# Kernel tuning notes

Hardware: AMD Instinct MI355X
Metric: run time of the kernel (lower is better)

Reference implementation:

```python
import jax, jax.numpy as jnp
import numpy as np

MARGIN = 0.3
N, D = 8192, 128
NUM_CLASSES = 512


def setup_inputs() -> dict:
    key = jax.random.key(0)
    k1, k2 = jax.random.split(key)
    embeddings = jax.random.normal(k1, (N, D), dtype=jnp.float32)
    targets = jax.random.randint(k2, (N,), 0, NUM_CLASSES, dtype=jnp.int64)
    return {"embeddings": embeddings, "targets": targets}


def reference(embeddings, targets):
    x = embeddings.astype(jnp.float32)
    # pairwise squared-euclidean: ||xi||^2 + ||xj||^2 - 2 xi.xj, clamped then sqrt
    sq = jnp.sum(x * x, axis=1)  # [N]
    dist = sq[:, None] + sq[None, :] - 2.0 * (x @ x.T)
    dist = jnp.sqrt(jnp.clip(dist, 1e-12, None))  # [N, N]

    is_pos = targets[:, None] == targets[None, :]  # includes diagonal, as in torch code

    # batch-hard mining: per-row hardest positive (max) and hardest negative (min)
    dist_ap = jnp.max(jnp.where(is_pos, dist, -jnp.inf), axis=1)
    dist_an = jnp.min(jnp.where(is_pos, jnp.inf, dist), axis=1)

    # MarginRankingLoss(margin)(dist_an, dist_ap, y=1) = mean(relu(margin - (dist_an - dist_ap)))
    loss = jnp.mean(jax.nn.relu(dist_ap - dist_an + MARGIN))
    return loss
```

## Files before the change

### kernel.cpp

```cpp
#include <hip/hip_runtime.h>
#include <hip/hip_bf16.h>

#define N_ROWS 8192
#define DIM 128
#define MARGIN_F 0.3f

typedef __attribute__((ext_vector_type(8))) short short8;
typedef __attribute__((ext_vector_type(4))) float f32x4;
typedef __attribute__((ext_vector_type(4))) int int4v;

typedef const void __attribute__((address_space(1)))* gas1_t;
typedef void __attribute__((address_space(3)))* las3_t;

__device__ __forceinline__ void load_lds16(const void* g, void* l) {
  __builtin_amdgcn_global_load_lds((gas1_t)g, (las3_t)l, 16, 0, 0);
}

__global__ __launch_bounds__(256) void prep_kernel(
    const float* __restrict__ x, const int* __restrict__ tgt,
    unsigned short* __restrict__ xb, float2* __restrict__ meta,
    int* __restrict__ apb, int* __restrict__ anb) {
  const int w = threadIdx.x >> 6, l = threadIdx.x & 63;
  const int row = blockIdx.x * 4 + w;
  const float2* xp = reinterpret_cast<const float2*>(x + (size_t)row * DIM);
  float2 v = xp[l];
  __hip_bfloat16 b0 = __float2bfloat16(v.x);
  __hip_bfloat16 b1 = __float2bfloat16(v.y);
  ushort2 st;
  st.x = *reinterpret_cast<unsigned short*>(&b0);
  st.y = *reinterpret_cast<unsigned short*>(&b1);
  reinterpret_cast<ushort2*>(xb)[(size_t)row * 64 + l] = st;
  float s = v.x * v.x + v.y * v.y;
  #pragma unroll
  for (int off = 32; off >= 1; off >>= 1) s += __shfl_xor(s, off);
  if (l == 0) {
    float2 m;
    m.x = s;
    m.y = __int_as_float(tgt[row]);
    meta[row] = m;
    apb[row] = 0x00000000;
    anb[row] = 0x7f800000;
  }
}

__global__ __launch_bounds__(256, 4) void gram_mine_kernel(
    const unsigned short* __restrict__ xb, const float2* __restrict__ meta,
    int* __restrict__ apb, int* __restrict__ anb) {
  __shared__ unsigned short Bs[2][64 * 128];

  const int t = threadIdx.x;
  const int w = t >> 6, l = t & 63;
  const int l15 = l & 15, l4 = l >> 4;
  const int rb = blockIdx.x * 128 + w * 32;
  const int chunkbase = blockIdx.y * 512;

  short8 a[2][4];
  #pragma unroll
  for (int rf = 0; rf < 2; ++rf) {
    const short8* p = reinterpret_cast<const short8*>(xb + (size_t)(rb + rf * 16 + l15) * DIM);
    #pragma unroll
    for (int kk = 0; kk < 4; ++kk) a[rf][kk] = p[kk * 4 + l4];
  }
  int t_r[8];
  #pragma unroll
  for (int rf = 0; rf < 2; ++rf)
    #pragma unroll
    for (int rg = 0; rg < 4; ++rg)
      t_r[rf * 4 + rg] = __float_as_int(meta[rb + rf * 16 + l4 * 4 + rg].y);

  float ap2[8], an2[8];
  #pragma unroll
  for (int i = 0; i < 8; ++i) { ap2[i] = -__builtin_inff(); an2[i] = __builtin_inff(); }

  auto stage = [&](int buf, int ct) {
    const int colbase = chunkbase + ct * 64;
    #pragma unroll
    for (int r = 0; r < 4; ++r) {
      int c = r * 256 + t;
      int col_local = c >> 4;
      int off = ((c & 15) * 16) ^ ((col_local & 7) << 4);
      const char* src = reinterpret_cast<const char*>(xb) +
                        (size_t)(colbase + col_local) * 256 + off;
      load_lds16(src, (char*)(&Bs[buf][0]) + c * 16);
    }
  };

  stage(0, 0);
  int cur = 0;
  for (int ct = 0; ct < 8; ++ct) {
    __syncthreads();
    if (ct < 7) stage(cur ^ 1, ct + 1);

    const int colbase = chunkbase + ct * 64;
    float sqc[4]; int tc[4];
    #pragma unroll
    for (int cf = 0; cf < 4; ++cf) {
      float2 m = meta[colbase + cf * 16 + l15];
      sqc[cf] = m.x; tc[cf] = __float_as_int(m.y);
    }

    f32x4 acc[2][4];
    #pragma unroll
    for (int rf = 0; rf < 2; ++rf)
      #pragma unroll
      for (int cf = 0; cf < 4; ++cf) acc[rf][cf] = (f32x4){0.f, 0.f, 0.f, 0.f};

    #pragma unroll
    for (int kk = 0; kk < 4; ++kk) {
      #pragma unroll
      for (int cf = 0; cf < 4; ++cf) {
        int col_local = cf * 16 + l15;
        int kb = (kk * 64 + l4 * 16) ^ ((col_local & 7) << 4);
        short8 b = *reinterpret_cast<const short8*>(
            reinterpret_cast<const char*>(&Bs[cur][0]) + col_local * 256 + kb);
        #pragma unroll
        for (int rf = 0; rf < 2; ++rf)
          acc[rf][cf] = __builtin_amdgcn_mfma_f32_16x16x32_bf16(
              a[rf][kk], b, acc[rf][cf], 0, 0, 0);
      }
    }

    #pragma unroll
    for (int cf = 0; cf < 4; ++cf) {
      #pragma unroll
      for (int rf = 0; rf < 2; ++rf)
        #pragma unroll
        for (int rg = 0; rg < 4; ++rg) {
          int idx = rf * 4 + rg;
          float v = fmaf(-2.f, acc[rf][cf][rg], sqc[cf]);
          bool pos = (t_r[idx] == tc[cf]);
          ap2[idx] = pos ? fmaxf(ap2[idx], v) : ap2[idx];
          an2[idx] = pos ? an2[idx] : fminf(an2[idx], v);
        }
    }
    cur ^= 1;
  }

  #pragma unroll
  for (int i = 0; i < 8; ++i) {
    #pragma unroll
    for (int off = 1; off < 16; off <<= 1) {
      ap2[i] = fmaxf(ap2[i], __shfl_xor(ap2[i], off));
      an2[i] = fminf(an2[i], __shfl_xor(an2[i], off));
    }
  }
  if (l15 == 0) {
    #pragma unroll
    for (int rf = 0; rf < 2; ++rf)
      #pragma unroll
      for (int rg = 0; rg < 4; ++rg) {
        int row = rb + rf * 16 + l4 * 4 + rg;
        float sqr = meta[row].x;
        float a2 = fmaxf(ap2[rf * 4 + rg] + sqr, 1e-12f);
        float n2 = fmaxf(an2[rf * 4 + rg] + sqr, 1e-12f);
        atomicMax(apb + row, __float_as_int(a2));
        atomicMin(anb + row, __float_as_int(n2));
      }
  }
}

__global__ __launch_bounds__(1024) void loss_kernel(
    const int4v* __restrict__ apb, const int4v* __restrict__ anb,
    float* __restrict__ out) {
  __shared__ float red[16];
  float s = 0.f;
  for (int i = threadIdx.x; i < N_ROWS / 4; i += 1024) {
    int4v a4 = apb[i], n4 = anb[i];
    #pragma unroll
    for (int j = 0; j < 4; ++j) {
      float ap = sqrtf(__int_as_float(a4[j]));
      float an = sqrtf(__int_as_float(n4[j]));
      float li = ap - an + MARGIN_F;
      s += li > 0.f ? li : 0.f;
    }
  }
  #pragma unroll
  for (int off = 32; off >= 1; off >>= 1) s += __shfl_xor(s, off);
  const int w = threadIdx.x >> 6, l = threadIdx.x & 63;
  if (l == 0) red[w] = s;
  __syncthreads();
  if (threadIdx.x < 16) {
    float v = red[threadIdx.x];
    #pragma unroll
    for (int off = 8; off >= 1; off >>= 1) v += __shfl_xor(v, off);
    if (threadIdx.x == 0) out[0] = v / (float)N_ROWS;
  }
}

extern "C" void kernel_launch(void* const* d_in, const int* in_sizes, int n_in,
                              void* d_out, int out_size, void* d_ws, size_t ws_size,
                              hipStream_t stream) {
  const float* x = (const float*)d_in[0];
  const int* tgt = (const int*)d_in[1];
  float* out = (float*)d_out;

  char* ws = (char*)d_ws;
  unsigned short* xb = (unsigned short*)ws;
  float2* meta = (float2*)(ws + 2097152);
  int* apb = (int*)(ws + 2097152 + 65536);
  int* anb = (int*)(ws + 2097152 + 65536 + 32768);

  prep_kernel<<<2048, 256, 0, stream>>>(x, tgt, xb, meta, apb, anb);
  gram_mine_kernel<<<dim3(64, 16), 256, 0, stream>>>(xb, meta, apb, anb);
  loss_kernel<<<1, 1024, 0, stream>>>((const int4v*)apb, (const int4v*)anb, out);
}
```

Before: 52.25 us.

## Store bf16 embeddings in MFMA fragment layout and load B directly from global

The prep kernel now writes the bf16 embeddings pre-swizzled into the per-lane MFMA 16x16x32 operand layout, so every lane's short8 fragment is contiguous and coalesced. The gram kernel drops the LDS double-buffered staging, the barriers and the XOR swizzle, and reads both A and B fragments straight from global memory (L2/L1). This removes the LDS traffic and synchronisation, but each of the 4 waves now fetches the same B tiles separately with no cross-wave reuse, and global load latency is no longer overlapped by explicit prefetch.

After: 51.30 us. Within noise of the previous version (-1.8%).

```diff
diff --git a/kernel.cpp b/kernel.cpp
--- a/kernel.cpp
+++ b/kernel.cpp
@@ -9,27 +9,22 @@
 typedef __attribute__((ext_vector_type(4))) float f32x4;
 typedef __attribute__((ext_vector_type(4))) int int4v;
 
-typedef const void __attribute__((address_space(1)))* gas1_t;
-typedef void __attribute__((address_space(3)))* las3_t;
-
-__device__ __forceinline__ void load_lds16(const void* g, void* l) {
-  __builtin_amdgcn_global_load_lds((gas1_t)g, (las3_t)l, 16, 0, 0);
-}
-
 __global__ __launch_bounds__(256) void prep_kernel(
     const float* __restrict__ x, const int* __restrict__ tgt,
-    unsigned short* __restrict__ xb, float2* __restrict__ meta,
+    unsigned short* __restrict__ xbB, float2* __restrict__ meta,
     int* __restrict__ apb, int* __restrict__ anb) {
   const int w = threadIdx.x >> 6, l = threadIdx.x & 63;
   const int row = blockIdx.x * 4 + w;
-  const float2* xp = reinterpret_cast<const float2*>(x + (size_t)row * DIM);
-  float2 v = xp[l];
+  float2 v = reinterpret_cast<const float2*>(x + (size_t)row * DIM)[l];
   __hip_bfloat16 b0 = __float2bfloat16(v.x);
   __hip_bfloat16 b1 = __float2bfloat16(v.y);
   ushort2 st;
   st.x = *reinterpret_cast<unsigned short*>(&b0);
   st.y = *reinterpret_cast<unsigned short*>(&b1);
-  reinterpret_cast<ushort2*>(xb)[(size_t)row * 64 + l] = st;
+  const int c16 = row >> 4, l15r = row & 15;
+  const int unit = c16 * 256 + (l >> 4) * 64 + ((l >> 2) & 3) * 16 + l15r;
+  reinterpret_cast<ushort2*>(xbB)[unit * 4 + (l & 3)] = st;
+
   float s = v.x * v.x + v.y * v.y;
   #pragma unroll
   for (int off = 32; off >= 1; off >>= 1) s += __shfl_xor(s, off);
@@ -44,23 +39,23 @@
 }
 
 __global__ __launch_bounds__(256, 4) void gram_mine_kernel(
-    const unsigned short* __restrict__ xb, const float2* __restrict__ meta,
+    const unsigned short* __restrict__ xbB, const float2* __restrict__ meta,
     int* __restrict__ apb, int* __restrict__ anb) {
-  __shared__ unsigned short Bs[2][64 * 128];
-
   const int t = threadIdx.x;
   const int w = t >> 6, l = t & 63;
   const int l15 = l & 15, l4 = l >> 4;
   const int rb = blockIdx.x * 128 + w * 32;
   const int chunkbase = blockIdx.y * 512;
 
+  const short8* xf = reinterpret_cast<const short8*>(xbB);
+
   short8 a[2][4];
   #pragma unroll
-  for (int rf = 0; rf < 2; ++rf) {
-    const short8* p = reinterpret_cast<const short8*>(xb + (size_t)(rb + rf * 16 + l15) * DIM);
+  for (int rf = 0; rf < 2; ++rf)
     #pragma unroll
-    for (int kk = 0; kk < 4; ++kk) a[rf][kk] = p[kk * 4 + l4];
-  }
+    for (int kk = 0; kk < 4; ++kk)
+      a[rf][kk] = xf[(rb >> 4 << 8) + rf * 256 + kk * 64 + l];
+
   int t_r[8];
   #pragma unroll
   for (int rf = 0; rf < 2; ++rf)
@@ -72,26 +67,10 @@
   #pragma unroll
   for (int i = 0; i < 8; ++i) { ap2[i] = -__builtin_inff(); an2[i] = __builtin_inff(); }
 
-  auto stage = [&](int buf, int ct) {
+  for (int ct = 0; ct < 8; ++ct) {
     const int colbase = chunkbase + ct * 64;
-    #pragma unroll
-    for (int r = 0; r < 4; ++r) {
-      int c = r * 256 + t;
-      int col_local = c >> 4;
-      int off = ((c & 15) * 16) ^ ((col_local & 7) << 4);
-      const char* src = reinterpret_cast<const char*>(xb) +
-                        (size_t)(colbase + col_local) * 256 + off;
-      load_lds16(src, (char*)(&Bs[buf][0]) + c * 16);
-    }
-  };
+    const int cb16 = colbase >> 4;
 
-  stage(0, 0);
-  int cur = 0;
-  for (int ct = 0; ct < 8; ++ct) {
-    __syncthreads();
-    if (ct < 7) stage(cur ^ 1, ct + 1);
-
-    const int colbase = chunkbase + ct * 64;
     float sqc[4]; int tc[4];
     #pragma unroll
     for (int cf = 0; cf < 4; ++cf) {
@@ -109,14 +88,9 @@
     for (int kk = 0; kk < 4; ++kk) {
       #pragma unroll
       for (int cf = 0; cf < 4; ++cf) {
-        int col_local = cf * 16 + l15;
-        int kb = (kk * 64 + l4 * 16) ^ ((col_local & 7) << 4);
-        short8 b = *reinterpret_cast<const short8*>(
-            reinterpret_cast<const char*>(&Bs[cur][0]) + col_local * 256 + kb);
-        #pragma unroll
-        for (int rf = 0; rf < 2; ++rf)
-          acc[rf][cf] = __builtin_amdgcn_mfma_f32_16x16x32_bf16(
-              a[rf][kk], b, acc[rf][cf], 0, 0, 0);
+        short8 b = xf[(cb16 + cf) * 256 + kk * 64 + l];
+        acc[0][cf] = __builtin_amdgcn_mfma_f32_16x16x32_bf16(a[0][kk], b, acc[0][cf], 0, 0, 0);
+        acc[1][cf] = __builtin_amdgcn_mfma_f32_16x16x32_bf16(a[1][kk], b, acc[1][cf], 0, 0, 0);
       }
     }
 
@@ -133,7 +107,6 @@
           an2[idx] = pos ? an2[idx] : fminf(an2[idx], v);
         }
     }
-    cur ^= 1;
   }
 
   #pragma unroll
@@ -195,12 +168,12 @@
   float* out = (float*)d_out;
 
   char* ws = (char*)d_ws;
-  unsigned short* xb = (unsigned short*)ws;
+  unsigned short* xbB = (unsigned short*)ws;
   float2* meta = (float2*)(ws + 2097152);
   int* apb = (int*)(ws + 2097152 + 65536);
   int* anb = (int*)(ws + 2097152 + 65536 + 32768);
 
-  prep_kernel<<<2048, 256, 0, stream>>>(x, tgt, xb, meta, apb, anb);
-  gram_mine_kernel<<<dim3(64, 16), 256, 0, stream>>>(xb, meta, apb, anb);
+  prep_kernel<<<2048, 256, 0, stream>>>(x, tgt, xbB, meta, apb, anb);
+  gram_mine_kernel<<<dim3(64, 16), 256, 0, stream>>>(xbB, meta, apb, anb);
   loss_kernel<<<1, 1024, 0, stream>>>((const int4v*)apb, (const int4v*)anb, out);
 }
```

## Fold -2 scale and column norms into MFMA, enlarge blocks, prefetch metadata

Applied to the files above, without the earlier changes.

Prep now writes a second bf16 copy of the embeddings, pre-scaled by -2 and stored in MFMA A-fragment order, so each row fragment loads as one contiguous coalesced read. The gram kernel seeds its accumulators with the column squared norms, which removes the per-element fma in the epilogue. Blocks grow to 512 threads covering 256 rows, so each staged B tile is shared by twice as many rows. Column metadata is prefetched one step ahead, MFMA sections run at raised wave priority, and the loop uses a single sync per step. The costs are an extra 2MB workspace write plus more register pressure, and bf16 rounding of -2x matches the old path exactly because scaling by a power of two is exact.

New measurement: 44.20 us. -15.4%, faster.

```diff
diff --git a/kernel.cpp b/kernel.cpp
--- a/kernel.cpp
+++ b/kernel.cpp
@@ -18,18 +18,25 @@
 
 __global__ __launch_bounds__(256) void prep_kernel(
     const float* __restrict__ x, const int* __restrict__ tgt,
-    unsigned short* __restrict__ xb, float2* __restrict__ meta,
-    int* __restrict__ apb, int* __restrict__ anb) {
+    unsigned short* __restrict__ xbA, unsigned short* __restrict__ xbBrow,
+    float2* __restrict__ meta, int* __restrict__ apb, int* __restrict__ anb) {
   const int w = threadIdx.x >> 6, l = threadIdx.x & 63;
   const int row = blockIdx.x * 4 + w;
-  const float2* xp = reinterpret_cast<const float2*>(x + (size_t)row * DIM);
-  float2 v = xp[l];
+  float2 v = reinterpret_cast<const float2*>(x + (size_t)row * DIM)[l];
   __hip_bfloat16 b0 = __float2bfloat16(v.x);
   __hip_bfloat16 b1 = __float2bfloat16(v.y);
-  ushort2 st;
-  st.x = *reinterpret_cast<unsigned short*>(&b0);
-  st.y = *reinterpret_cast<unsigned short*>(&b1);
-  reinterpret_cast<ushort2*>(xb)[(size_t)row * 64 + l] = st;
+  __hip_bfloat16 a0 = __float2bfloat16(-2.f * v.x);
+  __hip_bfloat16 a1 = __float2bfloat16(-2.f * v.y);
+  ushort2 stB, stA;
+  stB.x = *reinterpret_cast<unsigned short*>(&b0);
+  stB.y = *reinterpret_cast<unsigned short*>(&b1);
+  stA.x = *reinterpret_cast<unsigned short*>(&a0);
+  stA.y = *reinterpret_cast<unsigned short*>(&a1);
+  reinterpret_cast<ushort2*>(xbBrow)[(size_t)row * 64 + l] = stB;
+  const int c16 = row >> 4, l15r = row & 15;
+  const int unit = c16 * 256 + (l >> 4) * 64 + ((l >> 2) & 3) * 16 + l15r;
+  reinterpret_cast<ushort2*>(xbA)[unit * 4 + (l & 3)] = stA;
+
   float s = v.x * v.x + v.y * v.y;
   #pragma unroll
   for (int off = 32; off >= 1; off >>= 1) s += __shfl_xor(s, off);
@@ -43,24 +50,26 @@
   }
 }
 
-__global__ __launch_bounds__(256, 4) void gram_mine_kernel(
-    const unsigned short* __restrict__ xb, const float2* __restrict__ meta,
-    int* __restrict__ apb, int* __restrict__ anb) {
+__global__ __launch_bounds__(512, 4) void gram_mine_kernel(
+    const unsigned short* __restrict__ xbA, const unsigned short* __restrict__ xbBrow,
+    const float2* __restrict__ meta, int* __restrict__ apb, int* __restrict__ anb) {
   __shared__ unsigned short Bs[2][64 * 128];
 
   const int t = threadIdx.x;
   const int w = t >> 6, l = t & 63;
   const int l15 = l & 15, l4 = l >> 4;
-  const int rb = blockIdx.x * 128 + w * 32;
-  const int chunkbase = blockIdx.y * 512;
-
-  short8 a[2][4];
-  #pragma unroll
-  for (int rf = 0; rf < 2; ++rf) {
-    const short8* p = reinterpret_cast<const short8*>(xb + (size_t)(rb + rf * 16 + l15) * DIM);
-    #pragma unroll
-    for (int kk = 0; kk < 4; ++kk) a[rf][kk] = p[kk * 4 + l4];
-  }
+  const int rb = blockIdx.x * 256 + w * 32;
+  const int chunk = blockIdx.y * 512;
+
+  const short8* xfA = reinterpret_cast<const short8*>(xbA);
+
+  short8 a0[4], a1[4];
+  #pragma unroll
+  for (int kk = 0; kk < 4; ++kk) {
+    a0[kk] = xfA[(rb >> 4) * 256 + kk * 64 + l];
+    a1[kk] = xfA[((rb >> 4) + 1) * 256 + kk * 64 + l];
+  }
+
   int t_r[8];
   #pragma unroll
   for (int rf = 0; rf < 2; ++rf)
@@ -72,68 +81,81 @@
   #pragma unroll
   for (int i = 0; i < 8; ++i) { ap2[i] = -__builtin_inff(); an2[i] = __builtin_inff(); }
 
-  auto stage = [&](int buf, int ct) {
-    const int colbase = chunkbase + ct * 64;
-    #pragma unroll
-    for (int r = 0; r < 4; ++r) {
-      int c = r * 256 + t;
+  auto stage = [&](int buf, int s) {
+    const int colbase = chunk + s * 64;
+    #pragma unroll
+    for (int r = 0; r < 2; ++r) {
+      int c = r * 512 + t;
       int col_local = c >> 4;
       int off = ((c & 15) * 16) ^ ((col_local & 7) << 4);
-      const char* src = reinterpret_cast<const char*>(xb) +
+      const char* src = reinterpret_cast<const char*>(xbBrow) +
                         (size_t)(colbase + col_local) * 256 + off;
       load_lds16(src, (char*)(&Bs[buf][0]) + c * 16);
     }
   };
 
   stage(0, 0);
-  int cur = 0;
-  for (int ct = 0; ct < 8; ++ct) {
-    __syncthreads();
-    if (ct < 7) stage(cur ^ 1, ct + 1);
-
-    const int colbase = chunkbase + ct * 64;
-    float sqc[4]; int tc[4];
+  float2 mcc[4], mcn[4];
+  #pragma unroll
+  for (int cf = 0; cf < 4; ++cf) mcc[cf] = meta[chunk + cf * 16 + l15];
+  __syncthreads();
+
+  int buf = 0;
+  #pragma unroll 1
+  for (int s = 0; s < 8; ++s) {
+    if (s < 7) stage(buf ^ 1, s + 1);
+    const int ms = (s < 7) ? (s + 1) : s;
+    #pragma unroll
+    for (int cf = 0; cf < 4; ++cf) mcn[cf] = meta[chunk + ms * 64 + cf * 16 + l15];
+
+    f32x4 acc[2][4];
     #pragma unroll
     for (int cf = 0; cf < 4; ++cf) {
-      float2 m = meta[colbase + cf * 16 + l15];
-      sqc[cf] = m.x; tc[cf] = __float_as_int(m.y);
-    }
-
-    f32x4 acc[2][4];
-    #pragma unroll
-    for (int rf = 0; rf < 2; ++rf)
-      #pragma unroll
-      for (int cf = 0; cf < 4; ++cf) acc[rf][cf] = (f32x4){0.f, 0.f, 0.f, 0.f};
-
+      float s_ = mcc[cf].x;
+      f32x4 ci = {s_, s_, s_, s_};
+      acc[0][cf] = ci; acc[1][cf] = ci;
+    }
+
+    __builtin_amdgcn_s_setprio(1);
     #pragma unroll
     for (int kk = 0; kk < 4; ++kk) {
+      short8 b[4];
       #pragma unroll
       for (int cf = 0; cf < 4; ++cf) {
         int col_local = cf * 16 + l15;
         int kb = (kk * 64 + l4 * 16) ^ ((col_local & 7) << 4);
-        short8 b = *reinterpret_cast<const short8*>(
-            reinterpret_cast<const char*>(&Bs[cur][0]) + col_local * 256 + kb);
-        #pragma unroll
-        for (int rf = 0; rf < 2; ++rf)
-          acc[rf][cf] = __builtin_amdgcn_mfma_f32_16x16x32_bf16(
-              a[rf][kk], b, acc[rf][cf], 0, 0, 0);
+        b[cf] = *reinterpret_cast<const short8*>(
+            reinterpret_cast<const char*>(&Bs[buf][0]) + col_local * 256 + kb);
       }
-    }
+      #pragma unroll
+      for (int cf = 0; cf < 4; ++cf) {
+        acc[0][cf] = __builtin_amdgcn_mfma_f32_16x16x32_bf16(
+            a0[kk], b[cf], acc[0][cf], 0, 0, 0);
+        acc[1][cf] = __builtin_amdgcn_mfma_f32_16x16x32_bf16(
+            a1[kk], b[cf], acc[1][cf], 0, 0, 0);
+      }
+    }
+    __builtin_amdgcn_s_setprio(0);
 
     #pragma unroll
     for (int cf = 0; cf < 4; ++cf) {
+      const int tc = __float_as_int(mcc[cf].y);
       #pragma unroll
       for (int rf = 0; rf < 2; ++rf)
         #pragma unroll
         for (int rg = 0; rg < 4; ++rg) {
           int idx = rf * 4 + rg;
-          float v = fmaf(-2.f, acc[rf][cf][rg], sqc[cf]);
-          bool pos = (t_r[idx] == tc[cf]);
+          float v = acc[rf][cf][rg];
+          bool pos = (t_r[idx] == tc);
           ap2[idx] = pos ? fmaxf(ap2[idx], v) : ap2[idx];
           an2[idx] = pos ? an2[idx] : fminf(an2[idx], v);
         }
     }
-    cur ^= 1;
+
+    __syncthreads();
+    #pragma unroll
+    for (int cf = 0; cf < 4; ++cf) mcc[cf] = mcn[cf];
+    buf ^= 1;
   }
 
   #pragma unroll
@@ -195,12 +217,13 @@
   float* out = (float*)d_out;
 
   char* ws = (char*)d_ws;
-  unsigned short* xb = (unsigned short*)ws;
-  float2* meta = (float2*)(ws + 2097152);
-  int* apb = (int*)(ws + 2097152 + 65536);
-  int* anb = (int*)(ws + 2097152 + 65536 + 32768);
-
-  prep_kernel<<<2048, 256, 0, stream>>>(x, tgt, xb, meta, apb, anb);
-  gram_mine_kernel<<<dim3(64, 16), 256, 0, stream>>>(xb, meta, apb, anb);
+  unsigned short* xbA = (unsigned short*)ws;
+  unsigned short* xbBrow = (unsigned short*)(ws + 2097152);
+  float2* meta = (float2*)(ws + 4194304);
+  int* apb = (int*)(ws + 4194304 + 65536);
+  int* anb = (int*)(ws + 4194304 + 65536 + 32768);
+
+  prep_kernel<<<2048, 256, 0, stream>>>(x, tgt, xbA, xbBrow, meta, apb, anb);
+  gram_mine_kernel<<<dim3(32, 16), 512, 0, stream>>>(xbA, xbBrow, meta, apb, anb);
   loss_kernel<<<1, 1024, 0, stream>>>((const int4v*)apb, (const int4v*)anb, out);
 }
```
